# Kernel tuning notes

Measured on AMD Instinct MI355X. Metric: run time of the kernel, lower is better.

The kernel has to match this reference:

```python
import jax, jax.numpy as jnp
import numpy as np

N, T, V, F = 64, 5, 64, 256


def setup_inputs() -> dict:
    key = jax.random.key(0)
    k1, k2 = jax.random.split(key)
    x = jax.random.normal(k1, (N, T, V, F), dtype=jnp.float32)
    # keras 'uniform' initializer ~ U(-0.05, 0.05); keep positive-small for stable exp
    a = jax.random.uniform(k2, (F, 1), dtype=jnp.float32) * 0.05
    return {"x": x, "a": a}


def reference(x, a):
    # x: (N, T, V, F), a: (F, 1)
    t_mid = x.shape[1] // 2
    xm = x[:, t_mid]  # (N, V, F) -- middle time slice
    # pairwise L1 diffs: diff[n,i,j,f] = x[n,i,f] - x[n,j,f]
    absdiff = jnp.abs(xm[:, :, None, :] - xm[:, None, :, :])  # (N, V, V, F)
    # learned projection + exp: tmpS[n,i,j] = exp(sum_f |diff| * a[f])
    tmpS = jnp.exp(jnp.einsum('nijf,f->nij', absdiff, a[:, 0]))  # (N, V, V)
    # keras code divides by sum over axis=1 indexed at i (tmpS is symmetric)
    denom = jnp.sum(tmpS, axis=1)[:, :, None]  # (N, V, 1)
    return tmpS / denom
```

## Files before the change

kernel.cpp:

```cpp
#include <hip/hip_runtime.h>


#define NN 64
#define TT 5
#define VV 64
#define FF 256
#define TMID 2

__global__ void prescale_k(const float* __restrict__ x, const float* __restrict__ a,
                           float* __restrict__ y, int ynstride4) {
    int idx = blockIdx.x * 256 + threadIdx.x;
    int f4 = idx & 63;
    int j  = (idx >> 6) & 63;
    int n  = idx >> 12;
    const float4* xs = (const float4*)x;
    const float4* av = (const float4*)a;
    size_t src = ((size_t)(n * TT + TMID) * VV + j) * (FF / 4) + f4;
    float4 xv = xs[src];
    float4 s  = av[f4];
    const float L2E = 1.4426950408889634f;
    float4 o;
    o.x = xv.x * (s.x * L2E);
    o.y = xv.y * (s.y * L2E);
    o.z = xv.z * (s.z * L2E);
    o.w = xv.w * (s.w * L2E);
    ((float4*)y)[(size_t)n * ynstride4 + (j * (FF / 4)) + f4] = o;
}

__global__ __launch_bounds__(256) void pairnorm_k(const float* __restrict__ y,
                                                  float* __restrict__ out,
                                                  int ynstride4) {
    __shared__ float4 slab[VV * 64];

    const int tid  = threadIdx.x;
    const int lane = tid & 63;
    const int w    = tid >> 6;
    const int iq   = blockIdx.x;
    const int n    = blockIdx.y;

    const float4* ybase = (const float4*)y + (size_t)n * ynstride4;

    #pragma unroll
    for (int it = 0; it < 16; ++it) {
        int chunk = it * 256 + tid;
        int j = chunk >> 6;
        int c = chunk & 63;
        slab[(j << 6) + (c ^ (j & 7))] = ybase[chunk];
    }
    __syncthreads();

    const int i0 = __builtin_amdgcn_readfirstlane((iq << 4) + (w << 2));
    const float4* yi = ybase + (i0 << 6);

    float acc0 = 0.f, acc1 = 0.f, acc2 = 0.f, acc3 = 0.f;
    const int rb = lane << 6;
    const int s7 = lane & 7;

    #pragma unroll 4
    for (int c = 0; c < 64; ++c) {
        float4 xj = slab[rb + (c ^ s7)];
        float4 r0 = yi[c];
        float4 r1 = yi[64 + c];
        float4 r2 = yi[128 + c];
        float4 r3 = yi[192 + c];
        acc0 += (fabsf(r0.x - xj.x) + fabsf(r0.y - xj.y)) +
                (fabsf(r0.z - xj.z) + fabsf(r0.w - xj.w));
        acc1 += (fabsf(r1.x - xj.x) + fabsf(r1.y - xj.y)) +
                (fabsf(r1.z - xj.z) + fabsf(r1.w - xj.w));
        acc2 += (fabsf(r2.x - xj.x) + fabsf(r2.y - xj.y)) +
                (fabsf(r2.z - xj.z) + fabsf(r2.w - xj.w));
        acc3 += (fabsf(r3.x - xj.x) + fabsf(r3.y - xj.y)) +
                (fabsf(r3.z - xj.z) + fabsf(r3.w - xj.w));
    }

    float s0 = exp2f(acc0), s1 = exp2f(acc1), s2 = exp2f(acc2), s3 = exp2f(acc3);

    float d0 = s0, d1 = s1, d2 = s2, d3 = s3;
    #pragma unroll
    for (int m = 1; m < 64; m <<= 1) {
        d0 += __shfl_xor(d0, m, 64);
        d1 += __shfl_xor(d1, m, 64);
        d2 += __shfl_xor(d2, m, 64);
        d3 += __shfl_xor(d3, m, 64);
    }

    float* op = out + ((size_t)n * VV + i0) * VV + lane;
    op[0 * VV] = s0 / d0;
    op[1 * VV] = s1 / d1;
    op[2 * VV] = s2 / d2;
    op[3 * VV] = s3 / d3;
}

extern "C" void kernel_launch(void* const* d_in, const int* in_sizes, int n_in,
                              void* d_out, int out_size, void* d_ws, size_t ws_size,
                              hipStream_t stream) {
    const float* x = (const float*)d_in[0];
    const float* a = (const float*)d_in[1];
    float* out = (float*)d_out;

    const size_t y_bytes = (size_t)NN * VV * FF * sizeof(float);
    float* y;
    int ystr4;
    if (ws_size >= y_bytes) {
        y = (float*)d_ws;
        ystr4 = VV * FF / 4;
    } else {
        y = (float*)d_in[0];
        ystr4 = TT * VV * FF / 4;
    }

    hipLaunchKernelGGL(prescale_k, dim3(1024), dim3(256), 0, stream, x, a, y, ystr4);
    hipLaunchKernelGGL(pairnorm_k, dim3(4, 64), dim3(256), 0, stream, y, out, ystr4);
}
```

Baseline: 77.70 us.

## Fuse prescale into pairwise kernel and read row vectors from LDS

Drops the separate prescale kernel and its workspace round-trip. Each block now loads the middle time slice, scales it by a*log2e and stores it into swizzled LDS. The i-rows are read from LDS instead of global memory. The grid doubles to 8x64 blocks with two rows per wave instead of four, which raises parallelism. In exchange, every block redoes the 64KB load and scale, so global reads grow eightfold, though L2 should absorb most of that.

```diff
diff --git a/kernel.cpp b/kernel.cpp
--- a/kernel.cpp
+++ b/kernel.cpp
@@ -7,88 +7,65 @@
 #define FF 256
 #define TMID 2
 
-__global__ void prescale_k(const float* __restrict__ x, const float* __restrict__ a,
-                           float* __restrict__ y, int ynstride4) {
-    int idx = blockIdx.x * 256 + threadIdx.x;
-    int f4 = idx & 63;
-    int j  = (idx >> 6) & 63;
-    int n  = idx >> 12;
-    const float4* xs = (const float4*)x;
-    const float4* av = (const float4*)a;
-    size_t src = ((size_t)(n * TT + TMID) * VV + j) * (FF / 4) + f4;
-    float4 xv = xs[src];
-    float4 s  = av[f4];
-    const float L2E = 1.4426950408889634f;
-    float4 o;
-    o.x = xv.x * (s.x * L2E);
-    o.y = xv.y * (s.y * L2E);
-    o.z = xv.z * (s.z * L2E);
-    o.w = xv.w * (s.w * L2E);
-    ((float4*)y)[(size_t)n * ynstride4 + (j * (FF / 4)) + f4] = o;
-}
-
-__global__ __launch_bounds__(256) void pairnorm_k(const float* __restrict__ y,
-                                                  float* __restrict__ out,
-                                                  int ynstride4) {
+__global__ __launch_bounds__(256) void graphlearn_fused_k(const float* __restrict__ x,
+                                                          const float* __restrict__ a,
+                                                          float* __restrict__ out) {
     __shared__ float4 slab[VV * 64];
 
     const int tid  = threadIdx.x;
     const int lane = tid & 63;
     const int w    = tid >> 6;
-    const int iq   = blockIdx.x;
+    const int tile = blockIdx.x;
     const int n    = blockIdx.y;
 
-    const float4* ybase = (const float4*)y + (size_t)n * ynstride4;
+    const float L2E = 1.4426950408889634f;
+    float4 s = ((const float4*)a)[lane];
+    s.x *= L2E; s.y *= L2E; s.z *= L2E; s.w *= L2E;
 
+    const float4* xs = (const float4*)x + ((size_t)(n * TT + TMID) * VV) * (FF / 4);
     #pragma unroll
     for (int it = 0; it < 16; ++it) {
-        int chunk = it * 256 + tid;
-        int j = chunk >> 6;
-        int c = chunk & 63;
-        slab[(j << 6) + (c ^ (j & 7))] = ybase[chunk];
+        int j = it * 4 + w;
+        float4 xv = xs[(j << 6) + lane];
+        float4 o;
+        o.x = xv.x * s.x; o.y = xv.y * s.y; o.z = xv.z * s.z; o.w = xv.w * s.w;
+        slab[(j << 6) + (lane ^ (j & 7))] = o;
     }
     __syncthreads();
 
-    const int i0 = __builtin_amdgcn_readfirstlane((iq << 4) + (w << 2));
-    const float4* yi = ybase + (i0 << 6);
+    const int i0 = __builtin_amdgcn_readfirstlane((tile << 3) + (w << 1));
+    const int r0base = (i0 << 6);
+    const int r1base = ((i0 + 1) << 6);
+    const int x0 = i0 & 7;
+    const int x1 = (i0 + 1) & 7;
 
-    float acc0 = 0.f, acc1 = 0.f, acc2 = 0.f, acc3 = 0.f;
+    float acc0 = 0.f, acc1 = 0.f;
     const int rb = lane << 6;
     const int s7 = lane & 7;
 
-    #pragma unroll 4
+    #pragma unroll 8
     for (int c = 0; c < 64; ++c) {
         float4 xj = slab[rb + (c ^ s7)];
-        float4 r0 = yi[c];
-        float4 r1 = yi[64 + c];
-        float4 r2 = yi[128 + c];
-        float4 r3 = yi[192 + c];
+        float4 r0 = slab[r0base + (c ^ x0)];
+        float4 r1 = slab[r1base + (c ^ x1)];
         acc0 += (fabsf(r0.x - xj.x) + fabsf(r0.y - xj.y)) +
                 (fabsf(r0.z - xj.z) + fabsf(r0.w - xj.w));
         acc1 += (fabsf(r1.x - xj.x) + fabsf(r1.y - xj.y)) +
                 (fabsf(r1.z - xj.z) + fabsf(r1.w - xj.w));
-        acc2 += (fabsf(r2.x - xj.x) + fabsf(r2.y - xj.y)) +
-                (fabsf(r2.z - xj.z) + fabsf(r2.w - xj.w));
-        acc3 += (fabsf(r3.x - xj.x) + fabsf(r3.y - xj.y)) +
-                (fabsf(r3.z - xj.z) + fabsf(r3.w - xj.w));
     }
 
-    float s0 = exp2f(acc0), s1 = exp2f(acc1), s2 = exp2f(acc2), s3 = exp2f(acc3);
+    float s0 = exp2f(acc0), s1 = exp2f(acc1);
 
-    float d0 = s0, d1 = s1, d2 = s2, d3 = s3;
+    float d0 = s0, d1 = s1;
     #pragma unroll
     for (int m = 1; m < 64; m <<= 1) {
         d0 += __shfl_xor(d0, m, 64);
         d1 += __shfl_xor(d1, m, 64);
-        d2 += __shfl_xor(d2, m, 64);
-        d3 += __shfl_xor(d3, m, 64);
     }
 
     float* op = out + ((size_t)n * VV + i0) * VV + lane;
-    op[0 * VV] = s0 / d0;
-    op[1 * VV] = s1 / d1;
-    op[2 * VV] = s2 / d2;
-    op[3 * VV] = s3 / d3;
+    op[0]  = s0 / d0;
+    op[VV] = s1 / d1;
 }
 
 extern "C" void kernel_launch(void* const* d_in, const int* in_sizes, int n_in,
@@ -97,18 +74,8 @@
     const float* x = (const float*)d_in[0];
     const float* a = (const float*)d_in[1];
     float* out = (float*)d_out;
+    (void)d_ws; (void)ws_size;
 
-    const size_t y_bytes = (size_t)NN * VV * FF * sizeof(float);
-    float* y;
-    int ystr4;
-    if (ws_size >= y_bytes) {
-        y = (float*)d_ws;
-        ystr4 = VV * FF / 4;
-    } else {
-        y = (float*)d_in[0];
-        ystr4 = TT * VV * FF / 4;
-    }
-
-    hipLaunchKernelGGL(prescale_k, dim3(1024), dim3(256), 0, stream, x, a, y, ystr4);
-    hipLaunchKernelGGL(pairnorm_k, dim3(4, 64), dim3(256), 0, stream, y, out, ystr4);
+    hipLaunchKernelGGL(graphlearn_fused_k, dim3(8, 64), dim3(256), 0, stream,
+                       x, a, out);
 }
```

Result: faster. 75.56 us (-2.8%).
